# Optimization experiments

Measured on AMD Instinct MI355X. Metric: run time of the kernel, lower is better.

Reference implementation:

```python
import math
import jax, jax.numpy as jnp
import numpy as np

B, S, D, H = 2, 2048, 768, 12
DK = D // H  # 64
SCALE = math.sqrt(DK)


def setup_inputs() -> dict:
    key = jax.random.key(0)
    ks = jax.random.split(key, 8)
    q = jax.random.normal(ks[0], (B, S, D), dtype=jnp.float32)
    k = jax.random.normal(ks[1], (B, S, D), dtype=jnp.float32)
    v = jax.random.normal(ks[2], (B, S, D), dtype=jnp.float32)
    # causal mask (1 = attend, 0 = masked), per docstring [B, S, S]
    mask = jnp.broadcast_to(jnp.tril(jnp.ones((S, S), dtype=jnp.int32)), (B, S, S))
    std = 1.0 / math.sqrt(D)
    Wq = jax.random.uniform(ks[3], (D, D), jnp.float32, -std, std)
    Wk = jax.random.uniform(ks[4], (D, D), jnp.float32, -std, std)
    Wv = jax.random.uniform(ks[5], (D, D), jnp.float32, -std, std)
    Wo = jax.random.uniform(ks[6], (D, D), jnp.float32, -std, std)
    bo = jax.random.uniform(ks[7], (D,), jnp.float32, -std, std)
    return {"query": q, "key": k, "value": v, "mask": mask,
            "Wq": Wq, "Wk": Wk, "Wv": Wv, "Wo": Wo, "bo": bo}


def reference(query, key, value, mask, Wq, Wk, Wv, Wo, bo):
    # torch Linear: y = x @ W.T (no bias for q/k/v)
    Q = (query @ Wq.T).reshape(B, S, H, DK)  # [B,S,H,dk]
    K = (key @ Wk.T).reshape(B, S, H, DK)
    V = (value @ Wv.T).reshape(B, S, H, DK)
    # scores [B,H,S,S]
    scores = jnp.einsum('bqhd,bkhd->bhqk', Q, K) / SCALE
    scores = jnp.where(mask[:, None, :, :] == 0, jnp.float32(-1e9), scores)
    attention_weights = jax.nn.softmax(scores, axis=-1)
    # dropout is identity in eval mode (reference is deterministic)
    out = jnp.einsum('bhqk,bkhd->bqhd', attention_weights, V).reshape(B, S, D)
    output = out @ Wo.T + bo
    return output, attention_weights
```

## Files before the change

kernel.cpp:

```cpp
#include <hip/hip_runtime.h>
#include <cmath>

constexpr int B = 2, S = 2048, D = 768, H = 12, DK = 64;
constexpr int QKV_N = B * H * S * DK;
constexpr float INV_SCALE = 0.125f;


using bf16x8 = __attribute__((ext_vector_type(8))) short;
using f32x4  = __attribute__((ext_vector_type(4))) float;

#define DEVI __device__ __forceinline__

DEVI unsigned short f2hi(float x) { union { float f; unsigned u; } c; c.f = x; return (unsigned short)(c.u >> 16); }
DEVI float hi2f(unsigned short h) { union { unsigned u; float f; } c; c.u = (unsigned)h << 16; return c.f; }

DEVI void split8(const float* a, bf16x8& h8, bf16x8& l8) {
  #pragma unroll
  for (int i = 0; i < 8; i++) {
    unsigned short h = f2hi(a[i]);
    h8[i] = (short)h;
    l8[i] = (short)f2hi(a[i] - hi2f(h));
  }
}

DEVI f32x4 mfma3(bf16x8 ah, bf16x8 al, bf16x8 bh, bf16x8 bl, f32x4 acc) {
  acc = __builtin_amdgcn_mfma_f32_16x16x32_bf16(al, bh, acc, 0, 0, 0);
  acc = __builtin_amdgcn_mfma_f32_16x16x32_bf16(ah, bl, acc, 0, 0, 0);
  acc = __builtin_amdgcn_mfma_f32_16x16x32_bf16(ah, bh, acc, 0, 0, 0);
  return acc;
}

constexpr int PAD = 40;

__global__ __launch_bounds__(512)
void k_qkv_mfma(const float* __restrict__ Xq, const float* __restrict__ Xk,
                const float* __restrict__ Xv,
                const float* __restrict__ Wq, const float* __restrict__ Wk,
                const float* __restrict__ Wv,
                float* __restrict__ Qo, float* __restrict__ Ko, float* __restrict__ Vo) {
  __shared__ __align__(16) short Ah[128][PAD], Al[128][PAD];
  __shared__ __align__(16) short Bh[128][PAD], Bl[128][PAD];
  const int z = blockIdx.z;
  const float* __restrict__ X = (z == 0) ? Xq : (z == 1) ? Xk : Xv;
  const float* __restrict__ W = (z == 0) ? Wq : (z == 1) ? Wk : Wv;
  float* __restrict__ O = (z == 0) ? Qo : (z == 1) ? Ko : Vo;
  const float sc = (z == 0) ? INV_SCALE : 1.0f;
  const int m0 = blockIdx.y * 128, n0 = blockIdx.x * 128;
  const int t = threadIdx.x, wave = t >> 6, lane = t & 63;
  const int wm = (wave >> 1) * 32, wn = (wave & 1) * 64;
  const int srow = t >> 2, sch = (t & 3) * 8;
  const int fr = lane & 15, fk = (lane >> 4) * 8;

  f32x4 acc[2][4];
  #pragma unroll
  for (int i = 0; i < 2; i++)
    #pragma unroll
    for (int j = 0; j < 4; j++) acc[i][j] = (f32x4){0.f, 0.f, 0.f, 0.f};

  for (int k0 = 0; k0 < D; k0 += 32) {
    float abuf[8], bbuf[8];
    *(float4*)&abuf[0] = *(const float4*)&X[(size_t)(m0 + srow) * D + k0 + sch];
    *(float4*)&abuf[4] = *(const float4*)&X[(size_t)(m0 + srow) * D + k0 + sch + 4];
    *(float4*)&bbuf[0] = *(const float4*)&W[(size_t)(n0 + srow) * D + k0 + sch];
    *(float4*)&bbuf[4] = *(const float4*)&W[(size_t)(n0 + srow) * D + k0 + sch + 4];
    bf16x8 h8, l8;
    split8(abuf, h8, l8);
    *(bf16x8*)&Ah[srow][sch] = h8; *(bf16x8*)&Al[srow][sch] = l8;
    split8(bbuf, h8, l8);
    *(bf16x8*)&Bh[srow][sch] = h8; *(bf16x8*)&Bl[srow][sch] = l8;
    __syncthreads();
    bf16x8 a_h[2], a_l[2];
    #pragma unroll
    for (int st = 0; st < 2; st++) {
      a_h[st] = *(const bf16x8*)&Ah[wm + st * 16 + fr][fk];
      a_l[st] = *(const bf16x8*)&Al[wm + st * 16 + fr][fk];
    }
    #pragma unroll
    for (int ct = 0; ct < 4; ct++) {
      bf16x8 b_h = *(const bf16x8*)&Bh[wn + ct * 16 + fr][fk];
      bf16x8 b_l = *(const bf16x8*)&Bl[wn + ct * 16 + fr][fk];
      acc[0][ct] = mfma3(a_h[0], a_l[0], b_h, b_l, acc[0][ct]);
      acc[1][ct] = mfma3(a_h[1], a_l[1], b_h, b_l, acc[1][ct]);
    }
    __syncthreads();
  }
  #pragma unroll
  for (int st = 0; st < 2; st++)
    #pragma unroll
    for (int ct = 0; ct < 4; ct++)
      #pragma unroll
      for (int r = 0; r < 4; r++) {
        int m = m0 + wm + st * 16 + (lane >> 4) * 4 + r;
        int n = n0 + wn + ct * 16 + (lane & 15);
        int bb = m >> 11, ss = m & (S - 1), hh = n >> 6, dd = n & 63;
        O[(((size_t)bb * H + hh) * S + ss) * DK + dd] = acc[st][ct][r] * sc;
      }
}

__global__ __launch_bounds__(512)
void k_scores_mfma(const float* __restrict__ Q, const float* __restrict__ Kin,
                   float* __restrict__ attn) {
  const int kt = blockIdx.x, qt = blockIdx.y, bh = blockIdx.z;
  if (kt > qt) return;
  __shared__ __align__(16) short Ah[128][PAD], Al[128][PAD];
  __shared__ __align__(16) short Bh[128][PAD], Bl[128][PAD];
  const float* __restrict__ Qp = Q + (size_t)bh * S * DK;
  const float* __restrict__ Kp = Kin + (size_t)bh * S * DK;
  const int q0 = qt * 128, c0 = kt * 128;
  const int t = threadIdx.x, wave = t >> 6, lane = t & 63;
  const int wm = (wave >> 1) * 32, wn = (wave & 1) * 64;
  const int srow = t >> 2, sch = (t & 3) * 8;
  const int fr = lane & 15, fk = (lane >> 4) * 8;

  f32x4 acc[2][4];
  #pragma unroll
  for (int i = 0; i < 2; i++)
    #pragma unroll
    for (int j = 0; j < 4; j++) acc[i][j] = (f32x4){0.f, 0.f, 0.f, 0.f};

  for (int k0 = 0; k0 < DK; k0 += 32) {
    float abuf[8], bbuf[8];
    *(float4*)&abuf[0] = *(const float4*)&Qp[(size_t)(q0 + srow) * DK + k0 + sch];
    *(float4*)&abuf[4] = *(const float4*)&Qp[(size_t)(q0 + srow) * DK + k0 + sch + 4];
    *(float4*)&bbuf[0] = *(const float4*)&Kp[(size_t)(c0 + srow) * DK + k0 + sch];
    *(float4*)&bbuf[4] = *(const float4*)&Kp[(size_t)(c0 + srow) * DK + k0 + sch + 4];
    bf16x8 h8, l8;
    split8(abuf, h8, l8);
    *(bf16x8*)&Ah[srow][sch] = h8; *(bf16x8*)&Al[srow][sch] = l8;
    split8(bbuf, h8, l8);
    *(bf16x8*)&Bh[srow][sch] = h8; *(bf16x8*)&Bl[srow][sch] = l8;
    __syncthreads();
    bf16x8 a_h[2], a_l[2];
    #pragma unroll
    for (int st = 0; st < 2; st++) {
      a_h[st] = *(const bf16x8*)&Ah[wm + st * 16 + fr][fk];
      a_l[st] = *(const bf16x8*)&Al[wm + st * 16 + fr][fk];
    }
    #pragma unroll
    for (int ct = 0; ct < 4; ct++) {
      bf16x8 b_h = *(const bf16x8*)&Bh[wn + ct * 16 + fr][fk];
      bf16x8 b_l = *(const bf16x8*)&Bl[wn + ct * 16 + fr][fk];
      acc[0][ct] = mfma3(a_h[0], a_l[0], b_h, b_l, acc[0][ct]);
      acc[1][ct] = mfma3(a_h[1], a_l[1], b_h, b_l, acc[1][ct]);
    }
    __syncthreads();
  }
  #pragma unroll
  for (int st = 0; st < 2; st++)
    #pragma unroll
    for (int ct = 0; ct < 4; ct++)
      #pragma unroll
      for (int r = 0; r < 4; r++) {
        int qrow = q0 + wm + st * 16 + (lane >> 4) * 4 + r;
        int kcol = c0 + wn + ct * 16 + (lane & 15);
        attn[((size_t)bh * S + qrow) * S + kcol] =
            (kcol <= qrow) ? acc[st][ct][r] : -1e30f;
      }
}

__global__ __launch_bounds__(256)
void k_softmax(float* __restrict__ attn) {
  const int row = blockIdx.x;
  const int q = row & (S - 1);
  const int valid = q + 1;
  float* __restrict__ p = attn + (size_t)row * S;
  const int t = threadIdx.x;
  float v[8];
  if (t * 8 < valid) {
    float4 v0 = *(const float4*)&p[t * 8];
    float4 v1 = *(const float4*)&p[t * 8 + 4];
    v[0] = v0.x; v[1] = v0.y; v[2] = v0.z; v[3] = v0.w;
    v[4] = v1.x; v[5] = v1.y; v[6] = v1.z; v[7] = v1.w;
  } else {
    #pragma unroll
    for (int i = 0; i < 8; i++) v[i] = -3.0e38f;
  }
  float m = -3.0e38f;
  #pragma unroll
  for (int i = 0; i < 8; i++)
    if (t * 8 + i < valid) m = fmaxf(m, v[i]);
  #pragma unroll
  for (int o = 32; o > 0; o >>= 1) m = fmaxf(m, __shfl_xor(m, o));
  __shared__ float redm[4];
  __shared__ float redl[4];
  const int wid = t >> 6, lane = t & 63;
  if (lane == 0) redm[wid] = m;
  __syncthreads();
  m = fmaxf(fmaxf(redm[0], redm[1]), fmaxf(redm[2], redm[3]));
  float l = 0.f;
  #pragma unroll
  for (int i = 0; i < 8; i++) {
    float e = (t * 8 + i < valid) ? __expf(v[i] - m) : 0.f;
    v[i] = e; l += e;
  }
  #pragma unroll
  for (int o = 32; o > 0; o >>= 1) l += __shfl_xor(l, o);
  if (lane == 0) redl[wid] = l;
  __syncthreads();
  l = redl[0] + redl[1] + redl[2] + redl[3];
  const float inv = 1.0f / l;
  float4 s0, s1;
  s0.x = v[0] * inv; s0.y = v[1] * inv; s0.z = v[2] * inv; s0.w = v[3] * inv;
  s1.x = v[4] * inv; s1.y = v[5] * inv; s1.z = v[6] * inv; s1.w = v[7] * inv;
  *(float4*)&p[t * 8] = s0;
  *(float4*)&p[t * 8 + 4] = s1;
}

__global__ __launch_bounds__(512)
void k_pv_mfma(const float* __restrict__ attn, const float* __restrict__ V,
               float* __restrict__ ctx) {
  const int qt = blockIdx.x, bh = blockIdx.y;
  __shared__ __align__(16) short Ph[128][PAD], Pl[128][PAD];
  __shared__ __align__(16) short Vh[64][PAD], Vl[64][PAD];
  const float* __restrict__ Pp = attn + (size_t)bh * S * S;
  const float* __restrict__ Vp = V + (size_t)bh * S * DK;
  const int q0 = qt * 128;
  const int t = threadIdx.x, wave = t >> 6, lane = t & 63;
  const int wm = wave * 16;
  const int srow = t >> 2, sch = (t & 3) * 8;
  const int vk = t >> 4, vd = (t & 15) * 4;
  const int fr = lane & 15, fk = (lane >> 4) * 8;

  f32x4 acc[4];
  #pragma unroll
  for (int j = 0; j < 4; j++) acc[j] = (f32x4){0.f, 0.f, 0.f, 0.f};

  const int kend = (qt + 1) * 128;
  for (int k0 = 0; k0 < kend; k0 += 32) {
    float pbuf[8];
    *(float4*)&pbuf[0] = *(const float4*)&Pp[(size_t)(q0 + srow) * S + k0 + sch];
    *(float4*)&pbuf[4] = *(const float4*)&Pp[(size_t)(q0 + srow) * S + k0 + sch + 4];
    bf16x8 h8, l8;
    split8(pbuf, h8, l8);
    *(bf16x8*)&Ph[srow][sch] = h8; *(bf16x8*)&Pl[srow][sch] = l8;
    float4 vv = *(const float4*)&Vp[(size_t)(k0 + vk) * DK + vd];
    float va[4] = {vv.x, vv.y, vv.z, vv.w};
    #pragma unroll
    for (int i = 0; i < 4; i++) {
      unsigned short h = f2hi(va[i]);
      Vh[vd + i][vk] = (short)h;
      Vl[vd + i][vk] = (short)f2hi(va[i] - hi2f(h));
    }
    __syncthreads();
    bf16x8 a_h = *(const bf16x8*)&Ph[wm + fr][fk];
    bf16x8 a_l = *(const bf16x8*)&Pl[wm + fr][fk];
    #pragma unroll
    for (int ct = 0; ct < 4; ct++) {
      bf16x8 b_h = *(const bf16x8*)&Vh[ct * 16 + fr][fk];
      bf16x8 b_l = *(const bf16x8*)&Vl[ct * 16 + fr][fk];
      acc[ct] = mfma3(a_h, a_l, b_h, b_l, acc[ct]);
    }
    __syncthreads();
  }
  #pragma unroll
  for (int ct = 0; ct < 4; ct++)
    #pragma unroll
    for (int r = 0; r < 4; r++) {
      int qrow = q0 + wm + (lane >> 4) * 4 + r;
      int dcol = ct * 16 + (lane & 15);
      ctx[((size_t)bh * S + qrow) * DK + dcol] = acc[ct][r];
    }
}

__global__ __launch_bounds__(512)
void k_oproj_mfma(const float* __restrict__ ctx, const float* __restrict__ Wo,
                  const float* __restrict__ bo, float* __restrict__ out) {
  __shared__ __align__(16) short Ah[128][PAD], Al[128][PAD];
  __shared__ __align__(16) short Bh[128][PAD], Bl[128][PAD];
  const int m0 = blockIdx.y * 128, n0 = blockIdx.x * 128;
  const int t = threadIdx.x, wave = t >> 6, lane = t & 63;
  const int wm = (wave >> 1) * 32, wn = (wave & 1) * 64;
  const int srow = t >> 2, sch = (t & 3) * 8;
  const int fr = lane & 15, fk = (lane >> 4) * 8;

  f32x4 acc[2][4];
  #pragma unroll
  for (int i = 0; i < 2; i++)
    #pragma unroll
    for (int j = 0; j < 4; j++) acc[i][j] = (f32x4){0.f, 0.f, 0.f, 0.f};

  const int am = m0 + srow;
  const int abb = am >> 11, ass = am & (S - 1);
  for (int k0 = 0; k0 < D; k0 += 32) {
    float abuf[8], bbuf[8];
    int k = k0 + sch, hh = k >> 6, dd = k & 63;
    const float* pa = &ctx[(((size_t)abb * H + hh) * S + ass) * DK + dd];
    *(float4*)&abuf[0] = *(const float4*)&pa[0];
    *(float4*)&abuf[4] = *(const float4*)&pa[4];
    *(float4*)&bbuf[0] = *(const float4*)&Wo[(size_t)(n0 + srow) * D + k0 + sch];
    *(float4*)&bbuf[4] = *(const float4*)&Wo[(size_t)(n0 + srow) * D + k0 + sch + 4];
    bf16x8 h8, l8;
    split8(abuf, h8, l8);
    *(bf16x8*)&Ah[srow][sch] = h8; *(bf16x8*)&Al[srow][sch] = l8;
    split8(bbuf, h8, l8);
    *(bf16x8*)&Bh[srow][sch] = h8; *(bf16x8*)&Bl[srow][sch] = l8;
    __syncthreads();
    bf16x8 a_h[2], a_l[2];
    #pragma unroll
    for (int st = 0; st < 2; st++) {
      a_h[st] = *(const bf16x8*)&Ah[wm + st * 16 + fr][fk];
      a_l[st] = *(const bf16x8*)&Al[wm + st * 16 + fr][fk];
    }
    #pragma unroll
    for (int ct = 0; ct < 4; ct++) {
      bf16x8 b_h = *(const bf16x8*)&Bh[wn + ct * 16 + fr][fk];
      bf16x8 b_l = *(const bf16x8*)&Bl[wn + ct * 16 + fr][fk];
      acc[0][ct] = mfma3(a_h[0], a_l[0], b_h, b_l, acc[0][ct]);
      acc[1][ct] = mfma3(a_h[1], a_l[1], b_h, b_l, acc[1][ct]);
    }
    __syncthreads();
  }
  #pragma unroll
  for (int st = 0; st < 2; st++)
    #pragma unroll
    for (int ct = 0; ct < 4; ct++)
      #pragma unroll
      for (int r = 0; r < 4; r++) {
        int m = m0 + wm + st * 16 + (lane >> 4) * 4 + r;
        int n = n0 + wn + ct * 16 + (lane & 15);
        out[(size_t)m * D + n] = acc[st][ct][r] + bo[n];
      }
}

extern "C" void kernel_launch(void* const* d_in, const int* in_sizes, int n_in,
                              void* d_out, int out_size, void* d_ws, size_t ws_size,
                              hipStream_t stream) {
  (void)in_sizes; (void)n_in; (void)out_size; (void)ws_size;
  const float* q  = (const float*)d_in[0];
  const float* k  = (const float*)d_in[1];
  const float* v  = (const float*)d_in[2];
  const float* Wq = (const float*)d_in[4];
  const float* Wk = (const float*)d_in[5];
  const float* Wv = (const float*)d_in[6];
  const float* Wo = (const float*)d_in[7];
  const float* bo = (const float*)d_in[8];

  float* out  = (float*)d_out;
  float* attn = out + (size_t)B * S * D;

  float* ws  = (float*)d_ws;
  float* Qh  = ws;
  float* Kh  = ws + (size_t)QKV_N;
  float* Vh  = ws + (size_t)2 * QKV_N;
  float* ctx = ws + (size_t)3 * QKV_N;

  k_qkv_mfma<<<dim3(6, 32, 3), 512, 0, stream>>>(q, k, v, Wq, Wk, Wv, Qh, Kh, Vh);
  k_scores_mfma<<<dim3(16, 16, B * H), 512, 0, stream>>>(Qh, Kh, attn);
  k_softmax<<<dim3(B * H * S), 256, 0, stream>>>(attn);
  k_pv_mfma<<<dim3(16, B * H), 512, 0, stream>>>(attn, Vh, ctx);
  k_oproj_mfma<<<dim3(6, 32), 512, 0, stream>>>(ctx, Wo, bo, out);
}
```

Measured before the change: 829.8 us.

## Fuse scores, softmax and PV into a two-pass attention kernel with pre-split bf16 QKV

Replaces the separate scores, softmax and PV kernels with one kernel per 128-query tile. The first pass computes row max and sum online; the second recomputes scores, writes normalized probabilities once and accumulates P·V. The QKV projection now emits pre-split hi/lo bf16 halves, so the attention kernel skips per-load conversion, and the masked upper region is zero-filled directly. This removes the write-read-write round trips of the large attention matrix, at the cost of computing QK twice and launching a smaller grid (16x24 blocks) with reversed tile order for load balance.

```diff
diff --git a/kernel.cpp b/kernel.cpp
--- a/kernel.cpp
+++ b/kernel.cpp
@@ -7,6 +7,7 @@
 
 
 using bf16x8 = __attribute__((ext_vector_type(8))) short;
+using bf16x4 = __attribute__((ext_vector_type(4))) short;
 using f32x4  = __attribute__((ext_vector_type(4))) float;
 
 #define DEVI __device__ __forceinline__
@@ -23,12 +24,25 @@
   }
 }
 
-DEVI f32x4 mfma3(bf16x8 ah, bf16x8 al, bf16x8 bh, bf16x8 bl, f32x4 acc) {
+DEVI f32x4 mfma3_32(bf16x8 ah, bf16x8 al, bf16x8 bh, bf16x8 bl, f32x4 acc) {
   acc = __builtin_amdgcn_mfma_f32_16x16x32_bf16(al, bh, acc, 0, 0, 0);
   acc = __builtin_amdgcn_mfma_f32_16x16x32_bf16(ah, bl, acc, 0, 0, 0);
   acc = __builtin_amdgcn_mfma_f32_16x16x32_bf16(ah, bh, acc, 0, 0, 0);
   return acc;
 }
+
+#if __has_builtin(__builtin_amdgcn_mfma_f32_16x16x16bf16_1k)
+DEVI f32x4 mfma16(bf16x4 a, bf16x4 b, f32x4 c) { return __builtin_amdgcn_mfma_f32_16x16x16bf16_1k(a, b, c, 0, 0, 0); }
+#elif __has_builtin(__builtin_amdgcn_mfma_f32_16x16x16_bf16_1k)
+DEVI f32x4 mfma16(bf16x4 a, bf16x4 b, f32x4 c) { return __builtin_amdgcn_mfma_f32_16x16x16_bf16_1k(a, b, c, 0, 0, 0); }
+#elif __has_builtin(__builtin_amdgcn_mfma_f32_16x16x16_bf16)
+DEVI f32x4 mfma16(bf16x4 a, bf16x4 b, f32x4 c) { return __builtin_amdgcn_mfma_f32_16x16x16_bf16(a, b, c, 0, 0, 0); }
+#else
+DEVI f32x4 mfma16(bf16x4 a, bf16x4 b, f32x4 c) {
+  asm volatile("v_mfma_f32_16x16x16_bf16 %0, %1, %2, %0" : "+v"(c) : "v"(a), "v"(b));
+  return c;
+}
+#endif
 
 constexpr int PAD = 40;
 
@@ -37,13 +51,16 @@
                 const float* __restrict__ Xv,
                 const float* __restrict__ Wq, const float* __restrict__ Wk,
                 const float* __restrict__ Wv,
-                float* __restrict__ Qo, float* __restrict__ Ko, float* __restrict__ Vo) {
+                short* __restrict__ Qh, short* __restrict__ Ql,
+                short* __restrict__ Kh, short* __restrict__ Kl,
+                short* __restrict__ Vh, short* __restrict__ Vl) {
   __shared__ __align__(16) short Ah[128][PAD], Al[128][PAD];
   __shared__ __align__(16) short Bh[128][PAD], Bl[128][PAD];
   const int z = blockIdx.z;
   const float* __restrict__ X = (z == 0) ? Xq : (z == 1) ? Xk : Xv;
   const float* __restrict__ W = (z == 0) ? Wq : (z == 1) ? Wk : Wv;
-  float* __restrict__ O = (z == 0) ? Qo : (z == 1) ? Ko : Vo;
+  short* __restrict__ O_h = (z == 0) ? Qh : (z == 1) ? Kh : Vh;
+  short* __restrict__ O_l = (z == 0) ? Ql : (z == 1) ? Kl : Vl;
   const float sc = (z == 0) ? INV_SCALE : 1.0f;
   const int m0 = blockIdx.y * 128, n0 = blockIdx.x * 128;
   const int t = threadIdx.x, wave = t >> 6, lane = t & 63;
@@ -79,8 +96,8 @@
     for (int ct = 0; ct < 4; ct++) {
       bf16x8 b_h = *(const bf16x8*)&Bh[wn + ct * 16 + fr][fk];
       bf16x8 b_l = *(const bf16x8*)&Bl[wn + ct * 16 + fr][fk];
-      acc[0][ct] = mfma3(a_h[0], a_l[0], b_h, b_l, acc[0][ct]);
-      acc[1][ct] = mfma3(a_h[1], a_l[1], b_h, b_l, acc[1][ct]);
+      acc[0][ct] = mfma3_32(a_h[0], a_l[0], b_h, b_l, acc[0][ct]);
+      acc[1][ct] = mfma3_32(a_h[1], a_l[1], b_h, b_l, acc[1][ct]);
     }
     __syncthreads();
   }
@@ -92,174 +109,190 @@
       for (int r = 0; r < 4; r++) {
         int m = m0 + wm + st * 16 + (lane >> 4) * 4 + r;
         int n = n0 + wn + ct * 16 + (lane & 15);
-        int bb = m >> 11, ss = m & (S - 1), hh = n >> 6, dd = n & 63;
-        O[(((size_t)bb * H + hh) * S + ss) * DK + dd] = acc[st][ct][r] * sc;
-      }
-}
+        int bb = m >> 11, ss = m & (S - 1), hx = n >> 6, dd = n & 63;
+        size_t idx = (((size_t)bb * H + hx) * S + ss) * DK + dd;
+        float x = acc[st][ct][r] * sc;
+        unsigned short xh = f2hi(x);
+        O_h[idx] = (short)xh;
+        O_l[idx] = (short)f2hi(x - hi2f(xh));
+      }
+}
+
+constexpr int PADK = 80;
+constexpr int PADV = 136;
+constexpr int PADC = 132;
+constexpr int K_BYTES = 128 * PADK * 2;
+constexpr int V_BYTES = 64 * PADV * 2;
+constexpr int SMEM_BYTES = 2 * K_BYTES + 2 * V_BYTES;
 
 __global__ __launch_bounds__(512)
-void k_scores_mfma(const float* __restrict__ Q, const float* __restrict__ Kin,
-                   float* __restrict__ attn) {
-  const int kt = blockIdx.x, qt = blockIdx.y, bh = blockIdx.z;
-  if (kt > qt) return;
-  __shared__ __align__(16) short Ah[128][PAD], Al[128][PAD];
-  __shared__ __align__(16) short Bh[128][PAD], Bl[128][PAD];
-  const float* __restrict__ Qp = Q + (size_t)bh * S * DK;
-  const float* __restrict__ Kp = Kin + (size_t)bh * S * DK;
-  const int q0 = qt * 128, c0 = kt * 128;
+void k_attn_fused(const short* __restrict__ Qsh, const short* __restrict__ Qsl,
+                  const short* __restrict__ Ksg, const short* __restrict__ Klg,
+                  const short* __restrict__ Vsg, const short* __restrict__ Vlg,
+                  float* __restrict__ attn, float* __restrict__ ctx) {
+  __shared__ __align__(16) char smem[SMEM_BYTES];
+  short* Ksh = (short*)smem;
+  short* Ksl = (short*)(smem + K_BYTES);
+  short* VTh = (short*)(smem + 2 * K_BYTES);
+  short* VTl = (short*)(smem + 2 * K_BYTES + V_BYTES);
+  float* ctxT = (float*)smem;
+
+  const int qt = 15 - (int)blockIdx.x;
+  const int bh = blockIdx.y;
+  const int q0 = qt * 128;
+  const int kend = (qt + 1) * 128;
   const int t = threadIdx.x, wave = t >> 6, lane = t & 63;
-  const int wm = (wave >> 1) * 32, wn = (wave & 1) * 64;
-  const int srow = t >> 2, sch = (t & 3) * 8;
-  const int fr = lane & 15, fk = (lane >> 4) * 8;
-
-  f32x4 acc[2][4];
-  #pragma unroll
-  for (int i = 0; i < 2; i++)
-    #pragma unroll
-    for (int j = 0; j < 4; j++) acc[i][j] = (f32x4){0.f, 0.f, 0.f, 0.f};
-
-  for (int k0 = 0; k0 < DK; k0 += 32) {
-    float abuf[8], bbuf[8];
-    *(float4*)&abuf[0] = *(const float4*)&Qp[(size_t)(q0 + srow) * DK + k0 + sch];
-    *(float4*)&abuf[4] = *(const float4*)&Qp[(size_t)(q0 + srow) * DK + k0 + sch + 4];
-    *(float4*)&bbuf[0] = *(const float4*)&Kp[(size_t)(c0 + srow) * DK + k0 + sch];
-    *(float4*)&bbuf[4] = *(const float4*)&Kp[(size_t)(c0 + srow) * DK + k0 + sch + 4];
-    bf16x8 h8, l8;
-    split8(abuf, h8, l8);
-    *(bf16x8*)&Ah[srow][sch] = h8; *(bf16x8*)&Al[srow][sch] = l8;
-    split8(bbuf, h8, l8);
-    *(bf16x8*)&Bh[srow][sch] = h8; *(bf16x8*)&Bl[srow][sch] = l8;
-    __syncthreads();
-    bf16x8 a_h[2], a_l[2];
-    #pragma unroll
-    for (int st = 0; st < 2; st++) {
-      a_h[st] = *(const bf16x8*)&Ah[wm + st * 16 + fr][fk];
-      a_l[st] = *(const bf16x8*)&Al[wm + st * 16 + fr][fk];
-    }
-    #pragma unroll
-    for (int ct = 0; ct < 4; ct++) {
-      bf16x8 b_h = *(const bf16x8*)&Bh[wn + ct * 16 + fr][fk];
-      bf16x8 b_l = *(const bf16x8*)&Bl[wn + ct * 16 + fr][fk];
-      acc[0][ct] = mfma3(a_h[0], a_l[0], b_h, b_l, acc[0][ct]);
-      acc[1][ct] = mfma3(a_h[1], a_l[1], b_h, b_l, acc[1][ct]);
-    }
-    __syncthreads();
-  }
-  #pragma unroll
-  for (int st = 0; st < 2; st++)
-    #pragma unroll
-    for (int ct = 0; ct < 4; ct++)
-      #pragma unroll
-      for (int r = 0; r < 4; r++) {
-        int qrow = q0 + wm + st * 16 + (lane >> 4) * 4 + r;
-        int kcol = c0 + wn + ct * 16 + (lane & 15);
-        attn[((size_t)bh * S + qrow) * S + kcol] =
-            (kcol <= qrow) ? acc[st][ct][r] : -1e30f;
-      }
-}
-
-__global__ __launch_bounds__(256)
-void k_softmax(float* __restrict__ attn) {
-  const int row = blockIdx.x;
-  const int q = row & (S - 1);
-  const int valid = q + 1;
-  float* __restrict__ p = attn + (size_t)row * S;
-  const int t = threadIdx.x;
-  float v[8];
-  if (t * 8 < valid) {
-    float4 v0 = *(const float4*)&p[t * 8];
-    float4 v1 = *(const float4*)&p[t * 8 + 4];
-    v[0] = v0.x; v[1] = v0.y; v[2] = v0.z; v[3] = v0.w;
-    v[4] = v1.x; v[5] = v1.y; v[6] = v1.z; v[7] = v1.w;
-  } else {
-    #pragma unroll
-    for (int i = 0; i < 8; i++) v[i] = -3.0e38f;
-  }
-  float m = -3.0e38f;
-  #pragma unroll
-  for (int i = 0; i < 8; i++)
-    if (t * 8 + i < valid) m = fmaxf(m, v[i]);
-  #pragma unroll
-  for (int o = 32; o > 0; o >>= 1) m = fmaxf(m, __shfl_xor(m, o));
-  __shared__ float redm[4];
-  __shared__ float redl[4];
-  const int wid = t >> 6, lane = t & 63;
-  if (lane == 0) redm[wid] = m;
+  const int g = lane >> 4, c = lane & 15;
+  const int wq = wave * 16;
+  const int q = q0 + wq + c;
+  const size_t hrow = (size_t)bh * S;
+
+  {
+    const int ncols = S - kend;
+    if (ncols > 0) {
+      const float4 z4 = {0.f, 0.f, 0.f, 0.f};
+      for (int rr = 0; rr < 128; ++rr) {
+        float* rowp = &attn[(hrow + q0 + rr) * S + kend];
+        for (int cc = t * 4; cc < ncols; cc += 2048)
+          *(float4*)&rowp[cc] = z4;
+      }
+    }
+  }
+
+  bf16x8 qh0, ql0, qh1, ql1;
+  {
+    const size_t qb = (hrow + q) * DK + g * 8;
+    qh0 = *(const bf16x8*)&Qsh[qb];
+    ql0 = *(const bf16x8*)&Qsl[qb];
+    qh1 = *(const bf16x8*)&Qsh[qb + 32];
+    ql1 = *(const bf16x8*)&Qsl[qb + 32];
+  }
+
+  const int srow = t >> 2, sch = (t & 3) * 16;
+
+  float m_run = -3.0e38f, l_run = 0.f;
+  for (int kt = 0; kt <= qt; ++kt) {
+    {
+      const size_t gk = (hrow + (size_t)(kt * 128 + srow)) * DK + sch;
+      *(bf16x8*)&Ksh[srow * PADK + sch]     = *(const bf16x8*)&Ksg[gk];
+      *(bf16x8*)&Ksh[srow * PADK + sch + 8] = *(const bf16x8*)&Ksg[gk + 8];
+      *(bf16x8*)&Ksl[srow * PADK + sch]     = *(const bf16x8*)&Klg[gk];
+      *(bf16x8*)&Ksl[srow * PADK + sch + 8] = *(const bf16x8*)&Klg[gk + 8];
+    }
+    __syncthreads();
+    #pragma unroll
+    for (int f = 0; f < 8; ++f) {
+      const int krow = f * 16 + c;
+      bf16x8 kh0 = *(const bf16x8*)&Ksh[krow * PADK + g * 8];
+      bf16x8 kl0 = *(const bf16x8*)&Ksl[krow * PADK + g * 8];
+      bf16x8 kh1 = *(const bf16x8*)&Ksh[krow * PADK + 32 + g * 8];
+      bf16x8 kl1 = *(const bf16x8*)&Ksl[krow * PADK + 32 + g * 8];
+      f32x4 s = {0.f, 0.f, 0.f, 0.f};
+      s = mfma3_32(kh0, kl0, qh0, ql0, s);
+      s = mfma3_32(kh1, kl1, qh1, ql1, s);
+      const int kb = kt * 128 + f * 16 + g * 4;
+      float tm = -3.0e38f;
+      #pragma unroll
+      for (int r = 0; r < 4; ++r) {
+        float sv = (kb + r <= q) ? s[r] : -3.0e38f;
+        tm = fmaxf(tm, sv);
+      }
+      if (tm > m_run) { l_run *= __expf(m_run - tm); m_run = tm; }
+      #pragma unroll
+      for (int r = 0; r < 4; ++r)
+        l_run += (kb + r <= q) ? __expf(s[r] - m_run) : 0.f;
+    }
+    __syncthreads();
+  }
+  #pragma unroll
+  for (int off = 16; off <= 32; off <<= 1) {
+    float mo = __shfl_xor(m_run, off);
+    float lo2 = __shfl_xor(l_run, off);
+    float mn = fmaxf(m_run, mo);
+    l_run = l_run * __expf(m_run - mn) + lo2 * __expf(mo - mn);
+    m_run = mn;
+  }
+  const float inv_l = 1.0f / l_run;
+
+  f32x4 cacc[4];
+  #pragma unroll
+  for (int dt = 0; dt < 4; ++dt) cacc[dt] = (f32x4){0.f, 0.f, 0.f, 0.f};
+
+  for (int kt = 0; kt <= qt; ++kt) {
+    {
+      const size_t gk = (hrow + (size_t)(kt * 128 + srow)) * DK + sch;
+      *(bf16x8*)&Ksh[srow * PADK + sch]     = *(const bf16x8*)&Ksg[gk];
+      *(bf16x8*)&Ksh[srow * PADK + sch + 8] = *(const bf16x8*)&Ksg[gk + 8];
+      *(bf16x8*)&Ksl[srow * PADK + sch]     = *(const bf16x8*)&Klg[gk];
+      *(bf16x8*)&Ksl[srow * PADK + sch + 8] = *(const bf16x8*)&Klg[gk + 8];
+      bf16x8 vh0 = *(const bf16x8*)&Vsg[gk];
+      bf16x8 vh1 = *(const bf16x8*)&Vsg[gk + 8];
+      bf16x8 vl0 = *(const bf16x8*)&Vlg[gk];
+      bf16x8 vl1 = *(const bf16x8*)&Vlg[gk + 8];
+      #pragma unroll
+      for (int i = 0; i < 8; ++i) {
+        VTh[(sch + i) * PADV + srow]     = vh0[i];
+        VTh[(sch + 8 + i) * PADV + srow] = vh1[i];
+        VTl[(sch + i) * PADV + srow]     = vl0[i];
+        VTl[(sch + 8 + i) * PADV + srow] = vl1[i];
+      }
+    }
+    __syncthreads();
+    #pragma unroll
+    for (int f = 0; f < 8; ++f) {
+      const int krow = f * 16 + c;
+      bf16x8 kh0 = *(const bf16x8*)&Ksh[krow * PADK + g * 8];
+      bf16x8 kl0 = *(const bf16x8*)&Ksl[krow * PADK + g * 8];
+      bf16x8 kh1 = *(const bf16x8*)&Ksh[krow * PADK + 32 + g * 8];
+      bf16x8 kl1 = *(const bf16x8*)&Ksl[krow * PADK + 32 + g * 8];
+      f32x4 s = {0.f, 0.f, 0.f, 0.f};
+      s = mfma3_32(kh0, kl0, qh0, ql0, s);
+      s = mfma3_32(kh1, kl1, qh1, ql1, s);
+      const int kb = kt * 128 + f * 16 + g * 4;
+      float p[4];
+      #pragma unroll
+      for (int r = 0; r < 4; ++r) {
+        float e = __expf(s[r] - m_run) * inv_l;
+        p[r] = (kb + r <= q) ? e : 0.f;
+      }
+      float4 pw = {p[0], p[1], p[2], p[3]};
+      *(float4*)&attn[(hrow + q) * S + kb] = pw;
+      bf16x4 ph, pl;
+      #pragma unroll
+      for (int r = 0; r < 4; ++r) {
+        unsigned short xh = f2hi(p[r]);
+        ph[r] = (short)xh;
+        pl[r] = (short)f2hi(p[r] - hi2f(xh));
+      }
+      #pragma unroll
+      for (int dt = 0; dt < 4; ++dt) {
+        const int vr = dt * 16 + c;
+        bf16x4 vh4 = *(const bf16x4*)&VTh[vr * PADV + f * 16 + g * 4];
+        bf16x4 vl4 = *(const bf16x4*)&VTl[vr * PADV + f * 16 + g * 4];
+        cacc[dt] = mfma16(vl4, ph, cacc[dt]);
+        cacc[dt] = mfma16(vh4, pl, cacc[dt]);
+        cacc[dt] = mfma16(vh4, ph, cacc[dt]);
+      }
+    }
+    __syncthreads();
+  }
+
+  #pragma unroll
+  for (int dt = 0; dt < 4; ++dt)
+    #pragma unroll
+    for (int r = 0; r < 4; ++r)
+      ctxT[(dt * 16 + g * 4 + r) * PADC + wq + c] = cacc[dt][r];
   __syncthreads();
-  m = fmaxf(fmaxf(redm[0], redm[1]), fmaxf(redm[2], redm[3]));
-  float l = 0.f;
-  #pragma unroll
-  for (int i = 0; i < 8; i++) {
-    float e = (t * 8 + i < valid) ? __expf(v[i] - m) : 0.f;
-    v[i] = e; l += e;
-  }
-  #pragma unroll
-  for (int o = 32; o > 0; o >>= 1) l += __shfl_xor(l, o);
-  if (lane == 0) redl[wid] = l;
-  __syncthreads();
-  l = redl[0] + redl[1] + redl[2] + redl[3];
-  const float inv = 1.0f / l;
-  float4 s0, s1;
-  s0.x = v[0] * inv; s0.y = v[1] * inv; s0.z = v[2] * inv; s0.w = v[3] * inv;
-  s1.x = v[4] * inv; s1.y = v[5] * inv; s1.z = v[6] * inv; s1.w = v[7] * inv;
-  *(float4*)&p[t * 8] = s0;
-  *(float4*)&p[t * 8 + 4] = s1;
-}
-
-__global__ __launch_bounds__(512)
-void k_pv_mfma(const float* __restrict__ attn, const float* __restrict__ V,
-               float* __restrict__ ctx) {
-  const int qt = blockIdx.x, bh = blockIdx.y;
-  __shared__ __align__(16) short Ph[128][PAD], Pl[128][PAD];
-  __shared__ __align__(16) short Vh[64][PAD], Vl[64][PAD];
-  const float* __restrict__ Pp = attn + (size_t)bh * S * S;
-  const float* __restrict__ Vp = V + (size_t)bh * S * DK;
-  const int q0 = qt * 128;
-  const int t = threadIdx.x, wave = t >> 6, lane = t & 63;
-  const int wm = wave * 16;
-  const int srow = t >> 2, sch = (t & 3) * 8;
-  const int vk = t >> 4, vd = (t & 15) * 4;
-  const int fr = lane & 15, fk = (lane >> 4) * 8;
-
-  f32x4 acc[4];
-  #pragma unroll
-  for (int j = 0; j < 4; j++) acc[j] = (f32x4){0.f, 0.f, 0.f, 0.f};
-
-  const int kend = (qt + 1) * 128;
-  for (int k0 = 0; k0 < kend; k0 += 32) {
-    float pbuf[8];
-    *(float4*)&pbuf[0] = *(const float4*)&Pp[(size_t)(q0 + srow) * S + k0 + sch];
-    *(float4*)&pbuf[4] = *(const float4*)&Pp[(size_t)(q0 + srow) * S + k0 + sch + 4];
-    bf16x8 h8, l8;
-    split8(pbuf, h8, l8);
-    *(bf16x8*)&Ph[srow][sch] = h8; *(bf16x8*)&Pl[srow][sch] = l8;
-    float4 vv = *(const float4*)&Vp[(size_t)(k0 + vk) * DK + vd];
-    float va[4] = {vv.x, vv.y, vv.z, vv.w};
-    #pragma unroll
-    for (int i = 0; i < 4; i++) {
-      unsigned short h = f2hi(va[i]);
-      Vh[vd + i][vk] = (short)h;
-      Vl[vd + i][vk] = (short)f2hi(va[i] - hi2f(h));
-    }
-    __syncthreads();
-    bf16x8 a_h = *(const bf16x8*)&Ph[wm + fr][fk];
-    bf16x8 a_l = *(const bf16x8*)&Pl[wm + fr][fk];
-    #pragma unroll
-    for (int ct = 0; ct < 4; ct++) {
-      bf16x8 b_h = *(const bf16x8*)&Vh[ct * 16 + fr][fk];
-      bf16x8 b_l = *(const bf16x8*)&Vl[ct * 16 + fr][fk];
-      acc[ct] = mfma3(a_h, a_l, b_h, b_l, acc[ct]);
-    }
-    __syncthreads();
-  }
-  #pragma unroll
-  for (int ct = 0; ct < 4; ct++)
-    #pragma unroll
-    for (int r = 0; r < 4; r++) {
-      int qrow = q0 + wm + (lane >> 4) * 4 + r;
-      int dcol = ct * 16 + (lane & 15);
-      ctx[((size_t)bh * S + qrow) * DK + dcol] = acc[ct][r];
-    }
+  {
+    const int row = t >> 2, ch2 = (t & 3) * 16;
+    float buf[16];
+    #pragma unroll
+    for (int i = 0; i < 16; ++i) buf[i] = ctxT[(ch2 + i) * PADC + row];
+    float* cp = &ctx[(hrow + q0 + row) * DK + ch2];
+    #pragma unroll
+    for (int j = 0; j < 4; ++j)
+      *(float4*)&cp[j * 4] = *(const float4*)&buf[j * 4];
+  }
 }
 
 __global__ __launch_bounds__(512)
@@ -283,8 +316,8 @@
   const int abb = am >> 11, ass = am & (S - 1);
   for (int k0 = 0; k0 < D; k0 += 32) {
     float abuf[8], bbuf[8];
-    int k = k0 + sch, hh = k >> 6, dd = k & 63;
-    const float* pa = &ctx[(((size_t)abb * H + hh) * S + ass) * DK + dd];
+    int kk2 = k0 + sch, hx = kk2 >> 6, dd = kk2 & 63;
+    const float* pa = &ctx[(((size_t)abb * H + hx) * S + ass) * DK + dd];
     *(float4*)&abuf[0] = *(const float4*)&pa[0];
     *(float4*)&abuf[4] = *(const float4*)&pa[4];
     *(float4*)&bbuf[0] = *(const float4*)&Wo[(size_t)(n0 + srow) * D + k0 + sch];
@@ -305,8 +338,8 @@
     for (int ct = 0; ct < 4; ct++) {
       bf16x8 b_h = *(const bf16x8*)&Bh[wn + ct * 16 + fr][fk];
       bf16x8 b_l = *(const bf16x8*)&Bl[wn + ct * 16 + fr][fk];
-      acc[0][ct] = mfma3(a_h[0], a_l[0], b_h, b_l, acc[0][ct]);
-      acc[1][ct] = mfma3(a_h[1], a_l[1], b_h, b_l, acc[1][ct]);
+      acc[0][ct] = mfma3_32(a_h[0], a_l[0], b_h, b_l, acc[0][ct]);
+      acc[1][ct] = mfma3_32(a_h[1], a_l[1], b_h, b_l, acc[1][ct]);
     }
     __syncthreads();
   }
@@ -338,15 +371,16 @@
   float* out  = (float*)d_out;
   float* attn = out + (size_t)B * S * D;
 
-  float* ws  = (float*)d_ws;
-  float* Qh  = ws;
-  float* Kh  = ws + (size_t)QKV_N;
-  float* Vh  = ws + (size_t)2 * QKV_N;
-  float* ctx = ws + (size_t)3 * QKV_N;
-
-  k_qkv_mfma<<<dim3(6, 32, 3), 512, 0, stream>>>(q, k, v, Wq, Wk, Wv, Qh, Kh, Vh);
-  k_scores_mfma<<<dim3(16, 16, B * H), 512, 0, stream>>>(Qh, Kh, attn);
-  k_softmax<<<dim3(B * H * S), 256, 0, stream>>>(attn);
-  k_pv_mfma<<<dim3(16, B * H), 512, 0, stream>>>(attn, Vh, ctx);
+  short* Qh = (short*)d_ws;
+  short* Ql = Qh + (size_t)QKV_N;
+  short* Kh = Ql + (size_t)QKV_N;
+  short* Kl = Kh + (size_t)QKV_N;
+  short* Vh = Kl + (size_t)QKV_N;
+  short* Vl = Vh + (size_t)QKV_N;
+  float* ctx = (float*)(Vl + (size_t)QKV_N);
+
+  k_qkv_mfma<<<dim3(6, 32, 3), 512, 0, stream>>>(q, k, v, Wq, Wk, Wv,
+                                                 Qh, Ql, Kh, Kl, Vh, Vl);
+  k_attn_fused<<<dim3(16, 24), 512, 0, stream>>>(Qh, Ql, Kh, Kl, Vh, Vl, attn, ctx);
   k_oproj_mfma<<<dim3(6, 32), 512, 0, stream>>>(ctx, Wo, bo, out);
 }
```

After: 743.2 us. 10.4% less time.
